# Performance work log

Hardware: AMD Instinct MI355X
Metric: run time of the kernel (lower is better)

The kernel has to match this reference:

```python
import jax, jax.numpy as jnp
import numpy as np
import hashlib

# Model hyperparameters (from VictorASIFractalLightModel defaults)
B, L, D = 2, 2048, 1024
VOCAB, TOOL_VOCAB = 65536, 128
STEPS = 8            # FractalEmbedding steps -> 2*STEPS = 16 features
N_CONV, N_ATTN = 10, 6
HEADS, Q_GROUPS = 8, 2
HPG = HEADS // Q_GROUPS
HEAD_DIM = D // HEADS
KSIZE = 5
EPS = 1e-5


def _token_to_c(token_ids_np):
    # sha256-based complex constant per token id (exactly as in FractalEmbedding)
    flat = token_ids_np.reshape(-1)
    out = np.empty((flat.size, 2), dtype=np.float32)
    for i, tid in enumerate(flat):
        h = hashlib.sha256(str(int(tid)).encode()).hexdigest()
        out[i, 0] = (int(h[:16], 16) / 2**64 - 0.5) * 2.0
        out[i, 1] = (int(h[16:32], 16) / 2**64 - 0.5) * 2.0
    return out.reshape(token_ids_np.shape + (2,))


def _julia_feats(cs):
    # Vectorized julia iteration, z starts at 0.  cs: [B, L, 2] -> feats [B, L, 2*STEPS]
    cr, ci = cs[..., 0], cs[..., 1]
    zr = jnp.zeros_like(cr)
    zi = jnp.zeros_like(ci)
    feats = []
    for _ in range(STEPS):
        zr, zi = zr * zr - zi * zi + cr, 2.0 * zr * zi + ci
        feats.append(zr)
        feats.append(zi)
    return jnp.stack(feats, axis=-1)


def _layer_norm(x, s, b):
    mu = jnp.mean(x, axis=-1, keepdims=True)
    var = jnp.mean(jnp.square(x - mu), axis=-1, keepdims=True)
    return (x - mu) * jax.lax.rsqrt(var + EPS) * s + b


def _conv_block(x, dw_w, dw_b, pw_w, pw_b, ln_s, ln_b):
    # x: [B, L, D] -> depthwise conv (k=5, same pad) -> pointwise conv to 2D -> GLU -> residual LN
    xc = jnp.transpose(x, (0, 2, 1))  # [B, D, L]
    y = jax.lax.conv_general_dilated(xc, dw_w, (1,), [(KSIZE // 2, KSIZE // 2)],
                                     dimension_numbers=("NCH", "OIH", "NCH"),
                                     feature_group_count=D) + dw_b[None, :, None]
    y = jax.lax.conv_general_dilated(y, pw_w, (1,), [(0, 0)],
                                     dimension_numbers=("NCH", "OIH", "NCH")) + pw_b[None, :, None]
    y = jnp.transpose(y, (0, 2, 1))  # [B, L, 2D]
    a, gate = jnp.split(y, 2, axis=-1)
    return _layer_norm(x + a * jax.nn.sigmoid(gate), ln_s, ln_b)


def _attention(x, qw, kvw, ow, ln_s, ln_b):
    # Grouped-query attention with an explicit (unfused) score tensor, per the source.
    Bx, Lx, Dx = x.shape
    q = (x @ qw).reshape(Bx, Lx, Q_GROUPS, HPG, HEAD_DIM)
    kv = (x @ kvw).reshape(Bx, Lx, HEADS, 2, HEAD_DIM)
    k = kv[..., 0, :].reshape(Bx, Lx, Q_GROUPS, HPG, HEAD_DIM)
    v = kv[..., 1, :].reshape(Bx, Lx, Q_GROUPS, HPG, HEAD_DIM)
    scale = HEAD_DIM ** -0.5
    scores = jnp.einsum("bqghd,bkghd->bghqk", q, k) * scale  # [B, g, hpg, Lq, Lk]
    attn = jax.nn.softmax(scores, axis=-1)
    out = jnp.einsum("bghqk,bkghd->bqghd", attn, v).reshape(Bx, Lx, Dx)
    return _layer_norm(x + out @ ow, ln_s, ln_b)


def setup_inputs() -> dict:
    key = jax.random.key(0)
    ks = jax.random.split(key, 10)
    token_ids = jax.random.randint(ks[0], (B, L), 0, VOCAB)
    cs = jnp.asarray(_token_to_c(np.asarray(token_ids)))
    return {
        "token_ids": token_ids,
        "cs": cs,
        "proj_w": jax.random.normal(ks[1], (2 * STEPS, D), dtype=jnp.float32) * 0.25,
        "emb_scale": jnp.ones((1,), dtype=jnp.float32),
        "conv_dw_w": jax.random.normal(ks[2], (N_CONV, D, 1, KSIZE), dtype=jnp.float32) * 0.2,
        "conv_dw_b": jnp.zeros((N_CONV, D), dtype=jnp.float32),
        "conv_pw_w": jax.random.normal(ks[3], (N_CONV, 2 * D, D, 1), dtype=jnp.float32) * (D ** -0.5),
        "conv_pw_b": jnp.zeros((N_CONV, 2 * D), dtype=jnp.float32),
        "conv_ln_s": jnp.ones((N_CONV, D), dtype=jnp.float32),
        "conv_ln_b": jnp.zeros((N_CONV, D), dtype=jnp.float32),
        "attn_q_w": jax.random.normal(ks[4], (N_ATTN, D, D), dtype=jnp.float32) * (D ** -0.5),
        "attn_kv_w": jax.random.normal(ks[5], (N_ATTN, D, 2 * D), dtype=jnp.float32) * (D ** -0.5),
        "attn_out_w": jax.random.normal(ks[6], (N_ATTN, D, D), dtype=jnp.float32) * (D ** -0.5),
        "attn_ln_s": jnp.ones((N_ATTN, D), dtype=jnp.float32),
        "attn_ln_b": jnp.zeros((N_ATTN, D), dtype=jnp.float32),
        "lm_w": jax.random.normal(ks[7], (D, VOCAB), dtype=jnp.float32) * (D ** -0.5),
        "tool_w": jax.random.normal(ks[8], (D, TOOL_VOCAB), dtype=jnp.float32) * (D ** -0.5),
        "tool_b": jnp.zeros((TOOL_VOCAB,), dtype=jnp.float32),
    }


def reference(token_ids, cs, proj_w, emb_scale, conv_dw_w, conv_dw_b, conv_pw_w, conv_pw_b,
              conv_ln_s, conv_ln_b, attn_q_w, attn_kv_w, attn_out_w, attn_ln_s, attn_ln_b,
              lm_w, tool_w, tool_b):
    feats = _julia_feats(cs)                 # [B, L, 16]
    h = (feats @ proj_w) * emb_scale         # FractalEmbedding
    for i in range(N_CONV):
        h = _conv_block(h, conv_dw_w[i], conv_dw_b[i], conv_pw_w[i], conv_pw_b[i],
                        conv_ln_s[i], conv_ln_b[i])
    for i in range(N_ATTN):
        h = _attention(h, attn_q_w[i], attn_kv_w[i], attn_out_w[i], attn_ln_s[i], attn_ln_b[i])
    # ReplayMemoryStack is a side-effecting identity on h.
    last = h[:, -1, :]
    gen_logits = last @ lm_w
    tool_logits = last @ tool_w + tool_b
    return gen_logits, tool_logits
```

## Files before the change

### kernel.cpp

```cpp
#include <hip/hip_runtime.h>
#include <hip/hip_bf16.h>
#include <math.h>

#define B_ 2
#define L_ 2048
#define D_ 1024
#define VOCAB_ 65536
#define TOOLV_ 128
#define NCONV_ 10
#define NATTN_ 6
#define HEADS_ 8
#define HD_ 128
#define EPS_ 1e-5f

typedef short bf16x8 __attribute__((ext_vector_type(8)));
typedef short short4v __attribute__((ext_vector_type(4)));
typedef float f32x4 __attribute__((ext_vector_type(4)));
#define MFMA16(a,b,c) __builtin_amdgcn_mfma_f32_16x16x32_bf16(a, b, c, 0, 0, 0)

__device__ inline short f2bf(float f) {
  __hip_bfloat16 h = __float2bfloat16(f);
  return *reinterpret_cast<short*>(&h);
}

__device__ __forceinline__ void gld16(const void* g, void* l) {
  __builtin_amdgcn_global_load_lds(
      (const __attribute__((address_space(1))) unsigned int*)g,
      (__attribute__((address_space(3))) unsigned int*)l, 16, 0, 0);
}

__global__ __launch_bounds__(256) void julia_proj_k(const float* __restrict__ cs,
    const float* __restrict__ pw, const float* __restrict__ esc, float* __restrict__ h) {
  int row = blockIdx.x;
  float cr = cs[2*(size_t)row], ci = cs[2*(size_t)row+1];
  float f[16];
  float zr = 0.f, zi = 0.f;
  #pragma unroll
  for (int s = 0; s < 8; ++s) {
    float nzr = zr*zr - zi*zi + cr;
    float nzi = 2.f*zr*zi + ci;
    zr = nzr; zi = nzi;
    f[2*s] = zr; f[2*s+1] = zi;
  }
  float e = esc[0];
  for (int d = threadIdx.x; d < D_; d += 256) {
    float acc = 0.f;
    #pragma unroll
    for (int i = 0; i < 16; ++i) acc += f[i]*pw[i*D_ + d];
    h[(size_t)row*D_ + d] = acc*e;
  }
}

__global__ __launch_bounds__(256) void dwconv_k(const float* __restrict__ x,
    const float* __restrict__ w, const float* __restrict__ bias, short* __restrict__ y) {
  size_t idx = (size_t)blockIdx.x*256 + threadIdx.x;
  int d = (int)(idx & (D_-1));
  size_t bl = idx >> 10;
  int l = (int)(bl & (L_-1));
  size_t bbase = (bl >> 11) * (size_t)L_;
  float acc = bias[d];
  #pragma unroll
  for (int k = 0; k < 5; ++k) {
    int ll = l + k - 2;
    if (ll >= 0 && ll < L_)
      acc += x[(bbase + ll)*D_ + d] * w[d*5 + k];
  }
  y[idx] = f2bf(acc);
}

__global__ __launch_bounds__(256) void cvt_bf16_k(const float* __restrict__ x,
    short* __restrict__ y, int n4) {
  int i = blockIdx.x*256 + threadIdx.x;
  if (i >= n4) return;
  float4 v = ((const float4*)x)[i];
  short4v s = { f2bf(v.x), f2bf(v.y), f2bf(v.z), f2bf(v.w) };
  ((short4v*)y)[i] = s;
}

__global__ __launch_bounds__(256) void transp_bf16_k(const float* __restrict__ W0,
    short* __restrict__ WT0, int K, int N, size_t srcStride, size_t dstStride) {
  const float* W = W0 + blockIdx.z*srcStride;
  short* WT = WT0 + blockIdx.z*dstStride;
  __shared__ short t[32][33];
  int n0 = blockIdx.x*32, k0 = blockIdx.y*32;
  int tx = threadIdx.x & 31, ty = threadIdx.x >> 5;
  #pragma unroll
  for (int i = 0; i < 4; ++i) {
    int k = ty + i*8;
    t[tx][k] = f2bf(W[(size_t)(k0+k)*N + n0 + tx]);
  }
  __syncthreads();
  #pragma unroll
  for (int i = 0; i < 4; ++i) {
    int n = ty + i*8;
    WT[(size_t)(n0+n)*K + k0 + tx] = t[n][tx];
  }
}

template<int MODE, bool BIAS>
__global__ __launch_bounds__(256) void gemm_bf16(const short* __restrict__ A,
    const short* __restrict__ Bt, const float* __restrict__ bias,
    float* __restrict__ C, short* __restrict__ obf,
    short* __restrict__ kbf, short* __restrict__ vtbf,
    float scale, int M, int N, int K) {
  __shared__ short As[128*32];
  __shared__ short Bs[128*32];
  const int tid  = threadIdx.x;
  const int lane = tid & 63;
  const int wave = tid >> 6;
  const int wm = wave >> 1, wn = wave & 1;
  const int g = lane >> 4, c = lane & 15;
  const int m0 = blockIdx.x * 128, n0 = blockIdx.y * 128;

  f32x4 acc[4][4];
  #pragma unroll
  for (int i = 0; i < 4; ++i)
    #pragma unroll
    for (int j = 0; j < 4; ++j) acc[i][j] = (f32x4){0.f,0.f,0.f,0.f};

  const int srow = wave*16 + (lane>>2);
  const int scol = (lane&3)*8;
  const short* aSrc0 = A + (size_t)(m0 + srow)*K + scol;
  const short* aSrc1 = aSrc0 + (size_t)64*K;
  const short* bSrc0 = Bt + (size_t)(n0 + srow)*K + scol;
  const short* bSrc1 = bSrc0 + (size_t)64*K;
  short* AsW = &As[wave*512];
  short* BsW = &Bs[wave*512];

  for (int k0 = 0; k0 < K; k0 += 32) {
    __syncthreads();
    gld16(aSrc0 + k0, AsW);
    gld16(aSrc1 + k0, AsW + 2048);
    gld16(bSrc0 + k0, BsW);
    gld16(bSrc1 + k0, BsW + 2048);
    asm volatile("s_waitcnt vmcnt(0)" ::: "memory");
    __syncthreads();

    bf16x8 af[4], bfr[4];
    #pragma unroll
    for (int mi = 0; mi < 4; ++mi)
      af[mi] = *(const bf16x8*)&As[(wm*64 + mi*16 + c)*32 + g*8];
    #pragma unroll
    for (int ni = 0; ni < 4; ++ni)
      bfr[ni] = *(const bf16x8*)&Bs[(wn*64 + ni*16 + c)*32 + g*8];
    #pragma unroll
    for (int mi = 0; mi < 4; ++mi)
      #pragma unroll
      for (int ni = 0; ni < 4; ++ni)
        acc[mi][ni] = MFMA16(af[mi], bfr[ni], acc[mi][ni]);
  }

  #pragma unroll
  for (int mi = 0; mi < 4; ++mi) {
    int row = m0 + wm*64 + mi*16 + g*4;
    #pragma unroll
    for (int ni = 0; ni < 4; ++ni) {
      int col = n0 + wn*64 + ni*16 + c;
      if (MODE == 0) {
        float bv = BIAS ? bias[col] : 0.f;
        #pragma unroll
        for (int r = 0; r < 4; ++r)
          C[(size_t)(row+r)*N + col] = acc[mi][ni][r] + bv;
      } else {
        if (col < 1024) {
          #pragma unroll
          for (int r = 0; r < 4; ++r)
            obf[(size_t)(row+r)*1024 + col] = f2bf(acc[mi][ni][r]*scale);
        } else {
          int col2 = col - 1024;
          int hh = col2 >> 8, jj = (col2 >> 7) & 1, d = col2 & 127;
          int bb = row >> 11, l = row & 2047;
          size_t bh = (size_t)bb*8 + hh;
          if (jj == 0) {
            #pragma unroll
            for (int r = 0; r < 4; ++r)
              kbf[(bh*L_ + l + r)*128 + d] = f2bf(acc[mi][ni][r]);
          } else {
            #pragma unroll
            for (int r = 0; r < 4; ++r)
              vtbf[(bh*128 + d)*L_ + l + r] = f2bf(acc[mi][ni][r]);
          }
        }
      }
    }
  }
}

__global__ __launch_bounds__(256) void glu_ln_k(float* __restrict__ h,
    const float* __restrict__ y2, const float* __restrict__ s, const float* __restrict__ b,
    short* __restrict__ bo) {
  int row = blockIdx.x;
  int tid = threadIdx.x;
  float* xr = h + (size_t)row*D_;
  const float* yr = y2 + (size_t)row*2*D_;
  __shared__ float t[D_];
  __shared__ float red[256];
  float ls = 0.f;
  for (int d = tid; d < D_; d += 256) {
    float a = yr[d], g = yr[D_ + d];
    float sg = 1.f/(1.f + expf(-g));
    float v = xr[d] + a*sg;
    t[d] = v; ls += v;
  }
  red[tid] = ls; __syncthreads();
  for (int st = 128; st > 0; st >>= 1) { if (tid < st) red[tid] += red[tid+st]; __syncthreads(); }
  float mu = red[0] * (1.f/D_); __syncthreads();
  float lv = 0.f;
  for (int d = tid; d < D_; d += 256) { float dd = t[d]-mu; lv += dd*dd; }
  red[tid] = lv; __syncthreads();
  for (int st = 128; st > 0; st >>= 1) { if (tid < st) red[tid] += red[tid+st]; __syncthreads(); }
  float var = red[0] * (1.f/D_);
  float r = 1.f/sqrtf(var + EPS_);
  for (int d = tid; d < D_; d += 256) {
    float v = (t[d]-mu)*r*s[d] + b[d];
    xr[d] = v;
    if (bo) bo[(size_t)row*D_ + d] = f2bf(v);
  }
}

__global__ __launch_bounds__(256) void resid_ln_k(float* __restrict__ h,
    const float* __restrict__ proj, const float* __restrict__ s, const float* __restrict__ b,
    short* __restrict__ bo) {
  int row = blockIdx.x;
  int tid = threadIdx.x;
  float* xr = h + (size_t)row*D_;
  const float* pr = proj + (size_t)row*D_;
  __shared__ float t[D_];
  __shared__ float red[256];
  float ls = 0.f;
  for (int d = tid; d < D_; d += 256) { float v = xr[d] + pr[d]; t[d] = v; ls += v; }
  red[tid] = ls; __syncthreads();
  for (int st = 128; st > 0; st >>= 1) { if (tid < st) red[tid] += red[tid+st]; __syncthreads(); }
  float mu = red[0] * (1.f/D_); __syncthreads();
  float lv = 0.f;
  for (int d = tid; d < D_; d += 256) { float dd = t[d]-mu; lv += dd*dd; }
  red[tid] = lv; __syncthreads();
  for (int st = 128; st > 0; st >>= 1) { if (tid < st) red[tid] += red[tid+st]; __syncthreads(); }
  float var = red[0] * (1.f/D_);
  float r = 1.f/sqrtf(var + EPS_);
  for (int d = tid; d < D_; d += 256) {
    float v = (t[d]-mu)*r*s[d] + b[d];
    xr[d] = v;
    if (bo) bo[(size_t)row*D_ + d] = f2bf(v);
  }
}

#define PPITCH 72
__global__ __launch_bounds__(256) void attn2_k(const short* __restrict__ qbf,
    const short* __restrict__ kbf, const short* __restrict__ vtbf,
    short* __restrict__ obf) {
  __shared__ short Ks[64*128];
  __shared__ short Vts[128*64];
  __shared__ short Ps[4*16*PPITCH];

  const int tid  = threadIdx.x;
  const int wave = tid >> 6;
  const int lane = tid & 63;
  const int g    = lane >> 4;
  const int c    = lane & 15;
  const int hh   = blockIdx.y;
  const int b    = blockIdx.z;
  const int q0   = blockIdx.x*64 + wave*16;
  const size_t bh = (size_t)(b*HEADS_ + hh);

  bf16x8 qf[4];
  {
    const short* Qp = qbf + ((size_t)(b*L_ + q0 + c))*D_ + hh*HD_;
    #pragma unroll
    for (int kd = 0; kd < 4; ++kd)
      qf[kd] = *(const bf16x8*)(Qp + kd*32 + g*8);
  }

  f32x4 O[8];
  #pragma unroll
  for (int i = 0; i < 8; ++i) O[i] = (f32x4){0.f,0.f,0.f,0.f};
  float mrun[4] = {-INFINITY,-INFINITY,-INFINITY,-INFINITY};
  float lrun[4] = {0.f,0.f,0.f,0.f};
  short* Pw = Ps + wave*16*PPITCH;

  const short* kBase = kbf + bh*L_*128;
  const short* vBase = vtbf + bh*128*L_;

  for (int t = 0; t < L_/64; ++t) {
    __syncthreads();
    #pragma unroll
    for (int rd = 0; rd < 4; ++rd) {
      int slot = rd*256 + tid;
      int kr = slot >> 4, kj = slot & 15;
      int vr = slot >> 3, vj = slot & 7;
      gld16(kBase + ((size_t)(t*64 + kr))*128 + ((kj ^ (kr & 15)) * 8),
            (char*)Ks + (rd*256 + wave*64)*16);
      gld16(vBase + (size_t)vr*L_ + t*64 + ((vj ^ (vr & 7)) * 8),
            (char*)Vts + (rd*256 + wave*64)*16);
    }
    asm volatile("s_waitcnt vmcnt(0)" ::: "memory");
    __syncthreads();

    f32x4 s[4];
    #pragma unroll
    for (int nc = 0; nc < 4; ++nc) {
      s[nc] = (f32x4){0.f,0.f,0.f,0.f};
      int R = nc*16 + c;
      #pragma unroll
      for (int kd = 0; kd < 4; ++kd) {
        bf16x8 kf = *(const bf16x8*)&Ks[R*128 + (((kd*4 + g) ^ (R & 15)) * 8)];
        s[nc] = MFMA16(qf[kd], kf, s[nc]);
      }
    }

    float tm[4], rsum[4], alpha[4];
    #pragma unroll
    for (int r = 0; r < 4; ++r)
      tm[r] = fmaxf(fmaxf(s[0][r], s[1][r]), fmaxf(s[2][r], s[3][r]));
    #pragma unroll
    for (int r = 0; r < 4; ++r) {
      #pragma unroll
      for (int mask = 1; mask <= 8; mask <<= 1)
        tm[r] = fmaxf(tm[r], __shfl_xor(tm[r], mask));
      float mnew = fmaxf(mrun[r], tm[r]);
      alpha[r] = expf(mrun[r] - mnew);
      mrun[r] = mnew;
      rsum[r] = 0.f;
    }
    #pragma unroll
    for (int nc = 0; nc < 4; ++nc)
      #pragma unroll
      for (int r = 0; r < 4; ++r) {
        float p = expf(s[nc][r] - mrun[r]);
        s[nc][r] = p;
        rsum[r] += p;
      }
    #pragma unroll
    for (int r = 0; r < 4; ++r) {
      #pragma unroll
      for (int mask = 1; mask <= 8; mask <<= 1)
        rsum[r] += __shfl_xor(rsum[r], mask);
      lrun[r] = lrun[r]*alpha[r] + rsum[r];
    }
    #pragma unroll
    for (int nc = 0; nc < 8; ++nc)
      #pragma unroll
      for (int r = 0; r < 4; ++r) O[nc][r] *= alpha[r];

    #pragma unroll
    for (int nc = 0; nc < 4; ++nc)
      #pragma unroll
      for (int r = 0; r < 4; ++r)
        Pw[(g*4+r)*PPITCH + nc*16 + c] = f2bf(s[nc][r]);
    asm volatile("s_waitcnt lgkmcnt(0)" ::: "memory");
    bf16x8 pa0 = *(const bf16x8*)&Pw[c*PPITCH + g*8];
    bf16x8 pa1 = *(const bf16x8*)&Pw[c*PPITCH + 32 + g*8];

    #pragma unroll
    for (int ks = 0; ks < 2; ++ks) {
      #pragma unroll
      for (int nc = 0; nc < 8; ++nc) {
        int R = nc*16 + c;
        bf16x8 vf = *(const bf16x8*)&Vts[R*64 + (((ks*4 + g) ^ (R & 7)) * 8)];
        O[nc] = MFMA16(ks ? pa1 : pa0, vf, O[nc]);
      }
    }
  }

  short* ob = obf + ((size_t)(b*L_ + q0))*D_ + hh*HD_;
  #pragma unroll
  for (int r = 0; r < 4; ++r) {
    float inv = 1.f / lrun[r];
    #pragma unroll
    for (int nc = 0; nc < 8; ++nc)
      ob[(size_t)(g*4+r)*D_ + nc*16 + c] = f2bf(O[nc][r] * inv);
  }
}

__global__ __launch_bounds__(256) void lm_head_k(const float* __restrict__ h,
    const float* __restrict__ lm_w, float* __restrict__ out) {
  int tid = threadIdx.x;
  int n = blockIdx.x*256 + tid;
  __shared__ float last0[D_], last1[D_];
  const float* h0 = h + ((size_t)0*L_ + (L_-1))*D_;
  const float* h1 = h + ((size_t)1*L_ + (L_-1))*D_;
  for (int d = tid; d < D_; d += 256) { last0[d] = h0[d]; last1[d] = h1[d]; }
  __syncthreads();
  float a0 = 0.f, a1 = 0.f;
  for (int k = 0; k < D_; ++k) {
    float w = lm_w[(size_t)k*VOCAB_ + n];
    a0 += last0[k]*w; a1 += last1[k]*w;
  }
  out[n] = a0;
  out[(size_t)VOCAB_ + n] = a1;
}

__global__ __launch_bounds__(128) void tool_head_k(const float* __restrict__ h,
    const float* __restrict__ tw, const float* __restrict__ tb, float* __restrict__ out) {
  int b = blockIdx.x;
  int tid = threadIdx.x;
  __shared__ float last[D_];
  const float* hr = h + ((size_t)b*L_ + (L_-1))*D_;
  for (int d = tid; d < D_; d += 128) last[d] = hr[d];
  __syncthreads();
  float acc = tb[tid];
  for (int k = 0; k < D_; ++k) acc += last[k]*tw[(size_t)k*TOOLV_ + tid];
  out[(size_t)2*VOCAB_ + (size_t)b*TOOLV_ + tid] = acc;
}

extern "C" void kernel_launch(void* const* d_in, const int* in_sizes, int n_in,
                              void* d_out, int out_size, void* d_ws, size_t ws_size,
                              hipStream_t stream) {
  const float* cs        = (const float*)d_in[1];
  const float* proj_w    = (const float*)d_in[2];
  const float* emb_scale = (const float*)d_in[3];
  const float* conv_dw_w = (const float*)d_in[4];
  const float* conv_dw_b = (const float*)d_in[5];
  const float* conv_pw_w = (const float*)d_in[6];
  const float* conv_pw_b = (const float*)d_in[7];
  const float* conv_ln_s = (const float*)d_in[8];
  const float* conv_ln_b = (const float*)d_in[9];
  const float* attn_q_w  = (const float*)d_in[10];
  const float* attn_kv_w = (const float*)d_in[11];
  const float* attn_out_w= (const float*)d_in[12];
  const float* attn_ln_s = (const float*)d_in[13];
  const float* attn_ln_b = (const float*)d_in[14];
  const float* lm_w      = (const float*)d_in[15];
  const float* tool_w    = (const float*)d_in[16];
  const float* tool_b    = (const float*)d_in[17];

  const int M = B_*L_;
  float* h    = (float*)d_ws;
  float* buf2 = h    + (size_t)M*D_;
  short* kbf  = (short*)(buf2 + (size_t)M*2*D_);
  short* vtbf = kbf + (size_t)B_*HEADS_*L_*128;
  short* abf  = (short*)(vtbf + (size_t)B_*HEADS_*128*L_);
  short* wconv= abf + (size_t)M*D_;
  short* wqkv = wconv + (size_t)NCONV_*2*D_*D_;
  short* wout = wqkv + (size_t)NATTN_*3*D_*D_;
  short* qbf  = (short*)(buf2 + (size_t)M*D_);

  const float scale = 0.088388347648318447f;

  {
    int n4 = NCONV_*2*D_*D_/4;
    cvt_bf16_k<<<(n4 + 255)/256, 256, 0, stream>>>(conv_pw_w, wconv, n4);
    transp_bf16_k<<<dim3(D_/32, D_/32, NATTN_), 256, 0, stream>>>(
        attn_q_w, wqkv, D_, D_, (size_t)D_*D_, (size_t)3*D_*D_);
    transp_bf16_k<<<dim3((2*D_)/32, D_/32, NATTN_), 256, 0, stream>>>(
        attn_kv_w, wqkv + (size_t)D_*D_, D_, 2*D_, (size_t)D_*2*D_, (size_t)3*D_*D_);
    transp_bf16_k<<<dim3(D_/32, D_/32, NATTN_), 256, 0, stream>>>(
        attn_out_w, wout, D_, D_, (size_t)D_*D_, (size_t)D_*D_);
  }

  julia_proj_k<<<M, 256, 0, stream>>>(cs, proj_w, emb_scale, h);

  for (int i = 0; i < NCONV_; ++i) {
    dwconv_k<<<(M*D_)/256, 256, 0, stream>>>(h, conv_dw_w + (size_t)i*D_*5,
                                             conv_dw_b + (size_t)i*D_, abf);
    gemm_bf16<0, true><<<dim3(M/128, (2*D_)/128), 256, 0, stream>>>(
        abf, wconv + (size_t)i*2*D_*D_, conv_pw_b + (size_t)i*2*D_,
        buf2, nullptr, nullptr, nullptr, 1.f, M, 2*D_, D_);
    glu_ln_k<<<M, 256, 0, stream>>>(h, buf2, conv_ln_s + (size_t)i*D_,
                                    conv_ln_b + (size_t)i*D_,
                                    (i == NCONV_-1) ? abf : (short*)nullptr);
  }

  for (int i = 0; i < NATTN_; ++i) {
    gemm_bf16<3, false><<<dim3(M/128, (3*D_)/128), 256, 0, stream>>>(
        abf, wqkv + (size_t)i*3*D_*D_, nullptr, nullptr, qbf, kbf, vtbf,
        scale, M, 3*D_, D_);
    attn2_k<<<dim3(L_/64, HEADS_, B_), 256, 0, stream>>>(qbf, kbf, vtbf, abf);
    gemm_bf16<0, false><<<dim3(M/128, D_/128), 256, 0, stream>>>(
        abf, wout + (size_t)i*D_*D_, nullptr, buf2, nullptr, nullptr, nullptr,
        1.f, M, D_, D_);
    resid_ln_k<<<M, 256, 0, stream>>>(h, buf2, attn_ln_s + (size_t)i*D_,
                                      attn_ln_b + (size_t)i*D_,
                                      (i < NATTN_-1) ? abf : (short*)nullptr);
  }

  lm_head_k<<<dim3(VOCAB_/256, 1), 256, 0, stream>>>(h, lm_w, (float*)d_out);
  tool_head_k<<<B_, 128, 0, stream>>>(h, tool_w, tool_b, (float*)d_out);
}
```

Measured before the change: 2.008 ms.

## Vectorize elementwise kernels, deepen GEMM K-step, split-K the LM head

Switches julia projection, depthwise conv and both layer-norm kernels to float4 loads and stores, and drops the shared staging buffer in the layer norms by keeping values in registers. The GEMM now loads a 64-wide K slab per barrier pair instead of 32, which halves the number of synchronisations at the cost of double the LDS footprint. The LM head is split into four K partitions with vectorized weight reads, followed by a small reduction kernel that writes to an extra workspace region. Together these target memory bandwidth and barrier overhead, with added LDS pressure and one more kernel launch.

Measured after the change: 1.834 ms. 1.09x faster.

```diff
diff --git a/kernel.cpp b/kernel.cpp
--- a/kernel.cpp
+++ b/kernel.cpp
@@ -43,29 +43,41 @@
     f[2*s] = zr; f[2*s+1] = zi;
   }
   float e = esc[0];
-  for (int d = threadIdx.x; d < D_; d += 256) {
-    float acc = 0.f;
-    #pragma unroll
-    for (int i = 0; i < 16; ++i) acc += f[i]*pw[i*D_ + d];
-    h[(size_t)row*D_ + d] = acc*e;
-  }
+  int d = threadIdx.x * 4;
+  float4 acc = {0.f, 0.f, 0.f, 0.f};
+  #pragma unroll
+  for (int i = 0; i < 16; ++i) {
+    float4 pv = *(const float4*)(pw + i*D_ + d);
+    acc.x += f[i]*pv.x; acc.y += f[i]*pv.y; acc.z += f[i]*pv.z; acc.w += f[i]*pv.w;
+  }
+  acc.x *= e; acc.y *= e; acc.z *= e; acc.w *= e;
+  *(float4*)(h + (size_t)row*D_ + d) = acc;
 }
 
 __global__ __launch_bounds__(256) void dwconv_k(const float* __restrict__ x,
     const float* __restrict__ w, const float* __restrict__ bias, short* __restrict__ y) {
-  size_t idx = (size_t)blockIdx.x*256 + threadIdx.x;
-  int d = (int)(idx & (D_-1));
-  size_t bl = idx >> 10;
-  int l = (int)(bl & (L_-1));
-  size_t bbase = (bl >> 11) * (size_t)L_;
-  float acc = bias[d];
+  int idx = blockIdx.x*256 + threadIdx.x;
+  int d = (idx & (D_/4 - 1)) * 4;
+  int bl = idx >> 8;
+  int l = bl & (L_-1);
+  size_t bbase = (size_t)(bl >> 11) * L_;
+  float4 acc = *(const float4*)(bias + d);
+  float wr[4][5];
+  #pragma unroll
+  for (int j = 0; j < 4; ++j)
+    #pragma unroll
+    for (int k = 0; k < 5; ++k) wr[j][k] = w[(d+j)*5 + k];
   #pragma unroll
   for (int k = 0; k < 5; ++k) {
     int ll = l + k - 2;
-    if (ll >= 0 && ll < L_)
-      acc += x[(bbase + ll)*D_ + d] * w[d*5 + k];
-  }
-  y[idx] = f2bf(acc);
+    if (ll >= 0 && ll < L_) {
+      float4 xv = *(const float4*)(x + (bbase + ll)*D_ + d);
+      acc.x += xv.x*wr[0][k]; acc.y += xv.y*wr[1][k];
+      acc.z += xv.z*wr[2][k]; acc.w += xv.w*wr[3][k];
+    }
+  }
+  short4v o = { f2bf(acc.x), f2bf(acc.y), f2bf(acc.z), f2bf(acc.w) };
+  ((short4v*)y)[idx] = o;
 }
 
 __global__ __launch_bounds__(256) void cvt_bf16_k(const float* __restrict__ x,
@@ -103,8 +115,8 @@
     float* __restrict__ C, short* __restrict__ obf,
     short* __restrict__ kbf, short* __restrict__ vtbf,
     float scale, int M, int N, int K) {
-  __shared__ short As[128*32];
-  __shared__ short Bs[128*32];
+  __shared__ short As[2*128*32];
+  __shared__ short Bs[2*128*32];
   const int tid  = threadIdx.x;
   const int lane = tid & 63;
   const int wave = tid >> 6;
@@ -127,27 +139,34 @@
   short* AsW = &As[wave*512];
   short* BsW = &Bs[wave*512];
 
-  for (int k0 = 0; k0 < K; k0 += 32) {
+  for (int k0 = 0; k0 < K; k0 += 64) {
     __syncthreads();
-    gld16(aSrc0 + k0, AsW);
-    gld16(aSrc1 + k0, AsW + 2048);
-    gld16(bSrc0 + k0, BsW);
-    gld16(bSrc1 + k0, BsW + 2048);
+    gld16(aSrc0 + k0,      AsW);
+    gld16(aSrc1 + k0,      AsW + 2048);
+    gld16(aSrc0 + k0 + 32, AsW + 4096);
+    gld16(aSrc1 + k0 + 32, AsW + 6144);
+    gld16(bSrc0 + k0,      BsW);
+    gld16(bSrc1 + k0,      BsW + 2048);
+    gld16(bSrc0 + k0 + 32, BsW + 4096);
+    gld16(bSrc1 + k0 + 32, BsW + 6144);
     asm volatile("s_waitcnt vmcnt(0)" ::: "memory");
     __syncthreads();
 
-    bf16x8 af[4], bfr[4];
-    #pragma unroll
-    for (int mi = 0; mi < 4; ++mi)
-      af[mi] = *(const bf16x8*)&As[(wm*64 + mi*16 + c)*32 + g*8];
-    #pragma unroll
-    for (int ni = 0; ni < 4; ++ni)
-      bfr[ni] = *(const bf16x8*)&Bs[(wn*64 + ni*16 + c)*32 + g*8];
-    #pragma unroll
-    for (int mi = 0; mi < 4; ++mi)
+    #pragma unroll
+    for (int s = 0; s < 2; ++s) {
+      bf16x8 af[4], bfr[4];
+      #pragma unroll
+      for (int mi = 0; mi < 4; ++mi)
+        af[mi] = *(const bf16x8*)&As[s*4096 + (wm*64 + mi*16 + c)*32 + g*8];
       #pragma unroll
       for (int ni = 0; ni < 4; ++ni)
-        acc[mi][ni] = MFMA16(af[mi], bfr[ni], acc[mi][ni]);
+        bfr[ni] = *(const bf16x8*)&Bs[s*4096 + (wn*64 + ni*16 + c)*32 + g*8];
+      #pragma unroll
+      for (int mi = 0; mi < 4; ++mi)
+        #pragma unroll
+        for (int ni = 0; ni < 4; ++ni)
+          acc[mi][ni] = MFMA16(af[mi], bfr[ni], acc[mi][ni]);
+    }
   }
 
   #pragma unroll
@@ -191,30 +210,39 @@
     short* __restrict__ bo) {
   int row = blockIdx.x;
   int tid = threadIdx.x;
+  int d = tid*4;
   float* xr = h + (size_t)row*D_;
   const float* yr = y2 + (size_t)row*2*D_;
-  __shared__ float t[D_];
   __shared__ float red[256];
-  float ls = 0.f;
-  for (int d = tid; d < D_; d += 256) {
-    float a = yr[d], g = yr[D_ + d];
-    float sg = 1.f/(1.f + expf(-g));
-    float v = xr[d] + a*sg;
-    t[d] = v; ls += v;
-  }
-  red[tid] = ls; __syncthreads();
+  float4 xv = *(const float4*)(xr + d);
+  float4 av = *(const float4*)(yr + d);
+  float4 gv = *(const float4*)(yr + D_ + d);
+  float v[4];
+  v[0] = xv.x + av.x/(1.f + expf(-gv.x));
+  v[1] = xv.y + av.y/(1.f + expf(-gv.y));
+  v[2] = xv.z + av.z/(1.f + expf(-gv.z));
+  v[3] = xv.w + av.w/(1.f + expf(-gv.w));
+  red[tid] = v[0]+v[1]+v[2]+v[3]; __syncthreads();
   for (int st = 128; st > 0; st >>= 1) { if (tid < st) red[tid] += red[tid+st]; __syncthreads(); }
   float mu = red[0] * (1.f/D_); __syncthreads();
   float lv = 0.f;
-  for (int d = tid; d < D_; d += 256) { float dd = t[d]-mu; lv += dd*dd; }
+  #pragma unroll
+  for (int j = 0; j < 4; ++j) { float dd = v[j]-mu; lv += dd*dd; }
   red[tid] = lv; __syncthreads();
   for (int st = 128; st > 0; st >>= 1) { if (tid < st) red[tid] += red[tid+st]; __syncthreads(); }
   float var = red[0] * (1.f/D_);
   float r = 1.f/sqrtf(var + EPS_);
-  for (int d = tid; d < D_; d += 256) {
-    float v = (t[d]-mu)*r*s[d] + b[d];
-    xr[d] = v;
-    if (bo) bo[(size_t)row*D_ + d] = f2bf(v);
+  float4 sv = *(const float4*)(s + d);
+  float4 bv = *(const float4*)(b + d);
+  float4 o;
+  o.x = (v[0]-mu)*r*sv.x + bv.x;
+  o.y = (v[1]-mu)*r*sv.y + bv.y;
+  o.z = (v[2]-mu)*r*sv.z + bv.z;
+  o.w = (v[3]-mu)*r*sv.w + bv.w;
+  *(float4*)(xr + d) = o;
+  if (bo) {
+    short4v ob = { f2bf(o.x), f2bf(o.y), f2bf(o.z), f2bf(o.w) };
+    *(short4v*)(bo + (size_t)row*D_ + d) = ob;
   }
 }
 
@@ -223,25 +251,34 @@
     short* __restrict__ bo) {
   int row = blockIdx.x;
   int tid = threadIdx.x;
+  int d = tid*4;
   float* xr = h + (size_t)row*D_;
   const float* pr = proj + (size_t)row*D_;
-  __shared__ float t[D_];
   __shared__ float red[256];
-  float ls = 0.f;
-  for (int d = tid; d < D_; d += 256) { float v = xr[d] + pr[d]; t[d] = v; ls += v; }
-  red[tid] = ls; __syncthreads();
+  float4 xv = *(const float4*)(xr + d);
+  float4 pv = *(const float4*)(pr + d);
+  float v[4] = { xv.x+pv.x, xv.y+pv.y, xv.z+pv.z, xv.w+pv.w };
+  red[tid] = v[0]+v[1]+v[2]+v[3]; __syncthreads();
   for (int st = 128; st > 0; st >>= 1) { if (tid < st) red[tid] += red[tid+st]; __syncthreads(); }
   float mu = red[0] * (1.f/D_); __syncthreads();
   float lv = 0.f;
-  for (int d = tid; d < D_; d += 256) { float dd = t[d]-mu; lv += dd*dd; }
+  #pragma unroll
+  for (int j = 0; j < 4; ++j) { float dd = v[j]-mu; lv += dd*dd; }
   red[tid] = lv; __syncthreads();
   for (int st = 128; st > 0; st >>= 1) { if (tid < st) red[tid] += red[tid+st]; __syncthreads(); }
   float var = red[0] * (1.f/D_);
   float r = 1.f/sqrtf(var + EPS_);
-  for (int d = tid; d < D_; d += 256) {
-    float v = (t[d]-mu)*r*s[d] + b[d];
-    xr[d] = v;
-    if (bo) bo[(size_t)row*D_ + d] = f2bf(v);
+  float4 sv = *(const float4*)(s + d);
+  float4 bv = *(const float4*)(b + d);
+  float4 o;
+  o.x = (v[0]-mu)*r*sv.x + bv.x;
+  o.y = (v[1]-mu)*r*sv.y + bv.y;
+  o.z = (v[2]-mu)*r*sv.z + bv.z;
+  o.w = (v[3]-mu)*r*sv.w + bv.w;
+  *(float4*)(xr + d) = o;
+  if (bo) {
+    short4v ob = { f2bf(o.x), f2bf(o.y), f2bf(o.z), f2bf(o.w) };
+    *(short4v*)(bo + (size_t)row*D_ + d) = ob;
   }
 }
 
@@ -372,22 +409,40 @@
   }
 }
 
-__global__ __launch_bounds__(256) void lm_head_k(const float* __restrict__ h,
-    const float* __restrict__ lm_w, float* __restrict__ out) {
+__global__ __launch_bounds__(256) void lm_head_part_k(const float* __restrict__ h,
+    const float* __restrict__ lm_w, float* __restrict__ part) {
   int tid = threadIdx.x;
-  int n = blockIdx.x*256 + tid;
-  __shared__ float last0[D_], last1[D_];
-  const float* h0 = h + ((size_t)0*L_ + (L_-1))*D_;
-  const float* h1 = h + ((size_t)1*L_ + (L_-1))*D_;
-  for (int d = tid; d < D_; d += 256) { last0[d] = h0[d]; last1[d] = h1[d]; }
+  int n = (blockIdx.x*256 + tid)*4;
+  int ks = blockIdx.y;
+  __shared__ float last0[256], last1[256];
+  const float* h0 = h + ((size_t)0*L_ + (L_-1))*D_ + ks*256;
+  const float* h1 = h + ((size_t)1*L_ + (L_-1))*D_ + ks*256;
+  last0[tid] = h0[tid]; last1[tid] = h1[tid];
   __syncthreads();
-  float a0 = 0.f, a1 = 0.f;
-  for (int k = 0; k < D_; ++k) {
-    float w = lm_w[(size_t)k*VOCAB_ + n];
-    a0 += last0[k]*w; a1 += last1[k]*w;
-  }
-  out[n] = a0;
-  out[(size_t)VOCAB_ + n] = a1;
+  float4 a0 = {0.f,0.f,0.f,0.f}, a1 = {0.f,0.f,0.f,0.f};
+  const float* wp = lm_w + (size_t)(ks*256)*VOCAB_ + n;
+  for (int kk = 0; kk < 256; ++kk) {
+    float4 wv = *(const float4*)(wp + (size_t)kk*VOCAB_);
+    float c0 = last0[kk], c1 = last1[kk];
+    a0.x += c0*wv.x; a0.y += c0*wv.y; a0.z += c0*wv.z; a0.w += c0*wv.w;
+    a1.x += c1*wv.x; a1.y += c1*wv.y; a1.z += c1*wv.z; a1.w += c1*wv.w;
+  }
+  *(float4*)(part + ((size_t)ks*2 + 0)*VOCAB_ + n) = a0;
+  *(float4*)(part + ((size_t)ks*2 + 1)*VOCAB_ + n) = a1;
+}
+
+__global__ __launch_bounds__(256) void lm_head_red_k(const float* __restrict__ part,
+    float* __restrict__ out) {
+  int i = blockIdx.x*256 + threadIdx.x;
+  int j = (i*4) / VOCAB_;
+  int n = (i*4) & (VOCAB_-1);
+  float4 acc = {0.f,0.f,0.f,0.f};
+  #pragma unroll
+  for (int ks = 0; ks < 4; ++ks) {
+    float4 v = *(const float4*)(part + ((size_t)ks*2 + j)*VOCAB_ + n);
+    acc.x += v.x; acc.y += v.y; acc.z += v.z; acc.w += v.w;
+  }
+  *(float4*)(out + (size_t)j*VOCAB_ + n) = acc;
 }
 
 __global__ __launch_bounds__(128) void tool_head_k(const float* __restrict__ h,
@@ -433,6 +488,7 @@
   short* wconv= abf + (size_t)M*D_;
   short* wqkv = wconv + (size_t)NCONV_*2*D_*D_;
   short* wout = wqkv + (size_t)NATTN_*3*D_*D_;
+  float* lmpart = (float*)(wout + (size_t)NATTN_*D_*D_);
   short* qbf  = (short*)(buf2 + (size_t)M*D_);
 
   const float scale = 0.088388347648318447f;
@@ -451,8 +507,8 @@
   julia_proj_k<<<M, 256, 0, stream>>>(cs, proj_w, emb_scale, h);
 
   for (int i = 0; i < NCONV_; ++i) {
-    dwconv_k<<<(M*D_)/256, 256, 0, stream>>>(h, conv_dw_w + (size_t)i*D_*5,
-                                             conv_dw_b + (size_t)i*D_, abf);
+    dwconv_k<<<(M*D_/4)/256, 256, 0, stream>>>(h, conv_dw_w + (size_t)i*D_*5,
+                                               conv_dw_b + (size_t)i*D_, abf);
     gemm_bf16<0, true><<<dim3(M/128, (2*D_)/128), 256, 0, stream>>>(
         abf, wconv + (size_t)i*2*D_*D_, conv_pw_b + (size_t)i*2*D_,
         buf2, nullptr, nullptr, nullptr, 1.f, M, 2*D_, D_);
@@ -474,6 +530,7 @@
                                       (i < NATTN_-1) ? abf : (short*)nullptr);
   }
 
-  lm_head_k<<<dim3(VOCAB_/256, 1), 256, 0, stream>>>(h, lm_w, (float*)d_out);
+  lm_head_part_k<<<dim3(VOCAB_/1024, 4), 256, 0, stream>>>(h, lm_w, lmpart);
+  lm_head_red_k<<<(2*VOCAB_/4)/256, 256, 0, stream>>>(lmpart, (float*)d_out);
   tool_head_k<<<B_, 128, 0, stream>>>(h, tool_w, tool_b, (float*)d_out);
 }
```
